# Kernel optimization log

Hardware: AMD Instinct MI355X
Metric: run time of the kernel (lower is better)

## Reference

```python
import jax, jax.numpy as jnp
import numpy as np

B, T, C, H = 4, 4096, 1024, 64

def setup_inputs() -> dict:
    key = jax.random.key(0)
    k1, k2, k3, k4 = jax.random.split(key, 4)
    x = jax.random.normal(k1, (B, T, C), dtype=jnp.float32)
    # Linear(n_embed, head_size, bias=False), stored as [in, out] for x @ W
    s = 1.0 / np.sqrt(C)
    Wq = jax.random.uniform(k2, (C, H), dtype=jnp.float32, minval=-s, maxval=s)
    Wk = jax.random.uniform(k3, (C, H), dtype=jnp.float32, minval=-s, maxval=s)
    Wv = jax.random.uniform(k4, (C, H), dtype=jnp.float32, minval=-s, maxval=s)
    return {"x": x, "Wq": Wq, "Wk": Wk, "Wv": Wv}

def reference(x, Wq, Wk, Wv):
    Bn, Tn, Cn = x.shape
    q = x @ Wq  # [B,T,H]
    k = x @ Wk  # [B,T,H]
    v = x @ Wv  # [B,T,H]
    # NOTE: original scales by C**-0.5 (embedding dim), not head_size**-0.5
    wei = jnp.einsum('bqh,bkh->bqk', q, k) * (Cn ** -0.5)  # [B,T,T]
    causal = jnp.tril(jnp.ones((Tn, Tn), dtype=bool))
    wei = jnp.where(causal, wei, -jnp.inf)
    wei = jax.nn.softmax(wei, axis=-1)
    out = jnp.einsum('bqk,bkh->bqh', wei, v)  # [B,T,H]
    return out
```

## Files before the change

### kernel.cpp

```cpp
#include <hip/hip_runtime.h>
#include <hip/hip_bf16.h>


#define B_DIM 4
#define T_DIM 4096
#define C_DIM 1024
#define H_DIM 64
#define SCALE 0.03125f
#define KP 72

typedef __attribute__((ext_vector_type(8))) short bf8;
typedef __attribute__((ext_vector_type(4))) float f32x4;

__device__ __forceinline__ ushort f2bf(float f) {
    union { float f; uint u; } x; x.f = f;
    const uint u = x.u;
    return (ushort)((u + 0x7FFFu + ((u >> 16) & 1u)) >> 16);
}
__device__ __forceinline__ uint cvt_pk_bf16(float lo, float hi) {
    uint r;
    asm("v_cvt_pk_bf16_f32 %0, %1, %2" : "=v"(r) : "v"(lo), "v"(hi));
    return r;
}

__global__ __launch_bounds__(256) void wt_kernel(
    const float* __restrict__ Wq, const float* __restrict__ Wk,
    const float* __restrict__ Wv, ushort* __restrict__ wtg)
{
    const int id  = blockIdx.x * 256 + threadIdx.x;
    const int col = id >> 7;
    const int k8  = (id & 127) * 8;
    const int m   = col >> 6, lc = col & 63;
    const float* W = (m == 0) ? Wq : (m == 1) ? Wk : Wv;
    ushort o[8];
    #pragma unroll
    for (int i = 0; i < 8; ++i)
        o[i] = f2bf(W[(size_t)(k8 + i) * H_DIM + lc]);
    *(bf8*)&wtg[(size_t)col * C_DIM + k8] = *(bf8*)o;
}

__global__ __launch_bounds__(256) void qkv_mfma_kernel(
    const float* __restrict__ x, const ushort* __restrict__ wtg,
    ushort* __restrict__ qo, ushort* __restrict__ ko, ushort* __restrict__ vo)
{
    __shared__ ushort xs[64][KP];
    __shared__ ushort wts[192][KP];
    const int t    = threadIdx.x;
    const int lane = t & 63, wave = t >> 6;
    const int g    = lane >> 4, lid = lane & 15;
    const int wr   = wave >> 1, wc = wave & 1;
    const size_t r0 = (size_t)blockIdx.x * 64;

    f32x4 acc[2][6] = {};

    const int xrow = t >> 2, xcol = (t & 3) * 16;
    float4 xr[4];
    bf8 wreg[6];

    #pragma unroll
    for (int i = 0; i < 4; ++i)
        xr[i] = *(const float4*)&x[(r0 + xrow) * C_DIM + xcol + i * 4];
    #pragma unroll
    for (int it = 0; it < 6; ++it) {
        const int n = t + it * 256;
        wreg[it] = *(const bf8*)&wtg[(size_t)(n >> 3) * C_DIM + (n & 7) * 8];
    }

    for (int kc = 0; kc < C_DIM / 64; ++kc) {
        __syncthreads();
        {
            uint p[8];
            p[0] = cvt_pk_bf16(xr[0].x, xr[0].y); p[1] = cvt_pk_bf16(xr[0].z, xr[0].w);
            p[2] = cvt_pk_bf16(xr[1].x, xr[1].y); p[3] = cvt_pk_bf16(xr[1].z, xr[1].w);
            p[4] = cvt_pk_bf16(xr[2].x, xr[2].y); p[5] = cvt_pk_bf16(xr[2].z, xr[2].w);
            p[6] = cvt_pk_bf16(xr[3].x, xr[3].y); p[7] = cvt_pk_bf16(xr[3].z, xr[3].w);
            *(bf8*)&xs[xrow][xcol]     = *(bf8*)&p[0];
            *(bf8*)&xs[xrow][xcol + 8] = *(bf8*)&p[4];
            #pragma unroll
            for (int it = 0; it < 6; ++it) {
                const int n = t + it * 256;
                *(bf8*)&wts[n >> 3][(n & 7) * 8] = wreg[it];
            }
        }
        __syncthreads();
        if (kc + 1 < C_DIM / 64) {
            const int kb = (kc + 1) * 64;
            #pragma unroll
            for (int i = 0; i < 4; ++i)
                xr[i] = *(const float4*)&x[(r0 + xrow) * C_DIM + kb + xcol + i * 4];
            #pragma unroll
            for (int it = 0; it < 6; ++it) {
                const int n = t + it * 256;
                wreg[it] = *(const bf8*)&wtg[(size_t)(n >> 3) * C_DIM + kb + (n & 7) * 8];
            }
        }
        #pragma unroll
        for (int ks = 0; ks < 2; ++ks) {
            const bf8 a0 = *(const bf8*)&xs[wr * 32 + lid][ks * 32 + g * 8];
            const bf8 a1 = *(const bf8*)&xs[wr * 32 + 16 + lid][ks * 32 + g * 8];
            #pragma unroll
            for (int j = 0; j < 6; ++j) {
                const bf8 bb = *(const bf8*)&wts[(wc * 6 + j) * 16 + lid][ks * 32 + g * 8];
                acc[0][j] = __builtin_amdgcn_mfma_f32_16x16x32_bf16(a0, bb, acc[0][j], 0, 0, 0);
                acc[1][j] = __builtin_amdgcn_mfma_f32_16x16x32_bf16(a1, bb, acc[1][j], 0, 0, 0);
            }
        }
    }

    #pragma unroll
    for (int rt = 0; rt < 2; ++rt)
        #pragma unroll
        for (int j = 0; j < 6; ++j) {
            const int ct = wc * 6 + j;
            const int m  = ct >> 2, lc = (ct & 3) * 16 + lid;
            ushort* dst = (m == 0) ? qo : (m == 1) ? ko : vo;
            const float sc = (m == 0) ? SCALE : 1.f;
            #pragma unroll
            for (int r = 0; r < 4; ++r) {
                const size_t row = r0 + wr * 32 + rt * 16 + 4 * g + r;
                dst[row * H_DIM + lc] = f2bf(acc[rt][j][r] * sc);
            }
        }
}

__global__ __launch_bounds__(256) void flash_mfma_kernel(
    const ushort* __restrict__ q, const ushort* __restrict__ k,
    const ushort* __restrict__ v, float* __restrict__ pO,
    float* __restrict__ pm, float* __restrict__ pl,
    float* __restrict__ out, int S, int nslots, int direct)
{
    const int qt = 63 - blockIdx.y;
    const int c  = blockIdx.x;
    const int kt_begin = c * S;
    const int kt_end   = min((c + 1) * S, qt + 1);
    if (kt_begin >= kt_end) return;

    __shared__ ushort ks[64][KP];
    __shared__ ushort vt[64][KP];
    __shared__ ushort ps[4][16][KP];

    const int t    = threadIdx.x;
    const int lane = t & 63, wave = t >> 6;
    const int g    = lane >> 4, lid = lane & 15;
    const int b    = blockIdx.z;
    const int bq0  = qt * 64;
    const size_t base = (size_t)b * T_DIM * H_DIM;

    const size_t qoff = base + (size_t)(bq0 + wave * 16 + lid) * H_DIM;
    const bf8 qf0 = *(const bf8*)&q[qoff + g * 8];
    const bf8 qf1 = *(const bf8*)&q[qoff + 32 + g * 8];

    f32x4 o_acc[4] = {};
    float m_run = -1e30f, l_run = 0.f;

    const int krow = t >> 3, kcol = (t & 7) * 8;
    const int vj = (t & 31) * 2, vc = (t >> 5) * 8;
    bf8 kr0, kr1, vr0, vr1;
    {
        const int kg = kt_begin * 64;
        kr0 = *(const bf8*)&k[base + (size_t)(kg + krow) * H_DIM + kcol];
        kr1 = *(const bf8*)&k[base + (size_t)(kg + 32 + krow) * H_DIM + kcol];
        vr0 = *(const bf8*)&v[base + (size_t)(kg + vj) * H_DIM + vc];
        vr1 = *(const bf8*)&v[base + (size_t)(kg + vj + 1) * H_DIM + vc];
    }

    for (int kt64 = kt_begin; kt64 < kt_end; ++kt64) {
        __syncthreads();
        *(bf8*)&ks[krow][kcol]      = kr0;
        *(bf8*)&ks[32 + krow][kcol] = kr1;
        #pragma unroll
        for (int i = 0; i < 8; ++i) {
            const uint pk = (uint)(ushort)vr0[i] | ((uint)(ushort)vr1[i] << 16);
            *(uint*)&vt[vc + i][vj] = pk;
        }
        __syncthreads();
        if (kt64 + 1 < kt_end) {
            const int kg = (kt64 + 1) * 64;
            kr0 = *(const bf8*)&k[base + (size_t)(kg + krow) * H_DIM + kcol];
            kr1 = *(const bf8*)&k[base + (size_t)(kg + 32 + krow) * H_DIM + kcol];
            vr0 = *(const bf8*)&v[base + (size_t)(kg + vj) * H_DIM + vc];
            vr1 = *(const bf8*)&v[base + (size_t)(kg + vj + 1) * H_DIM + vc];
        }

        f32x4 st[4];
        #pragma unroll
        for (int kt = 0; kt < 4; ++kt) {
            const bf8 kf0 = *(const bf8*)&ks[kt * 16 + lid][g * 8];
            const bf8 kf1 = *(const bf8*)&ks[kt * 16 + lid][32 + g * 8];
            f32x4 a = {0.f, 0.f, 0.f, 0.f};
            a = __builtin_amdgcn_mfma_f32_16x16x32_bf16(kf0, qf0, a, 0, 0, 0);
            a = __builtin_amdgcn_mfma_f32_16x16x32_bf16(kf1, qf1, a, 0, 0, 0);
            st[kt] = a;
        }

        if (kt64 == qt) {
            const int qloc = wave * 16 + lid;
            #pragma unroll
            for (int kt = 0; kt < 4; ++kt)
                #pragma unroll
                for (int r = 0; r < 4; ++r)
                    if (kt * 16 + 4 * g + r > qloc) st[kt][r] = -1e30f;
        }

        float mx0 = fmaxf(fmaxf(st[0][0], st[0][1]), fmaxf(st[0][2], st[0][3]));
        float mx1 = fmaxf(fmaxf(st[1][0], st[1][1]), fmaxf(st[1][2], st[1][3]));
        float mx2 = fmaxf(fmaxf(st[2][0], st[2][1]), fmaxf(st[2][2], st[2][3]));
        float mx3 = fmaxf(fmaxf(st[3][0], st[3][1]), fmaxf(st[3][2], st[3][3]));
        float mx = fmaxf(fmaxf(mx0, mx1), fmaxf(mx2, mx3));
        mx = fmaxf(mx, __shfl_xor(mx, 16));
        mx = fmaxf(mx, __shfl_xor(mx, 32));
        const float mnew = fmaxf(m_run, mx);
        const float fsc  = __expf(m_run - mnew);
        m_run = mnew;
        float ls = 0.f;
        #pragma unroll
        for (int kt = 0; kt < 4; ++kt)
            #pragma unroll
            for (int r = 0; r < 4; ++r) {
                const float p = __expf(st[kt][r] - mnew);
                st[kt][r] = p;
                ls += p;
            }
        ls += __shfl_xor(ls, 16);
        ls += __shfl_xor(ls, 32);
        l_run = l_run * fsc + ls;

        #pragma unroll
        for (int kt = 0; kt < 4; ++kt) {
            uint2 w;
            w.x = cvt_pk_bf16(st[kt][0], st[kt][1]);
            w.y = cvt_pk_bf16(st[kt][2], st[kt][3]);
            *(uint2*)&ps[wave][lid][kt * 16 + 4 * g] = w;
        }

        float fb[4];
        #pragma unroll
        for (int r = 0; r < 4; ++r) fb[r] = __shfl(fsc, 4 * g + r);
        #pragma unroll
        for (int ht = 0; ht < 4; ++ht)
            #pragma unroll
            for (int r = 0; r < 4; ++r) o_acc[ht][r] *= fb[r];

        const bf8 pa0 = *(const bf8*)&ps[wave][lid][g * 8];
        const bf8 pa1 = *(const bf8*)&ps[wave][lid][32 + g * 8];
        #pragma unroll
        for (int ht = 0; ht < 4; ++ht) {
            const bf8 vb0 = *(const bf8*)&vt[ht * 16 + lid][g * 8];
            const bf8 vb1 = *(const bf8*)&vt[ht * 16 + lid][32 + g * 8];
            o_acc[ht] = __builtin_amdgcn_mfma_f32_16x16x32_bf16(pa0, vb0, o_acc[ht], 0, 0, 0);
            o_acc[ht] = __builtin_amdgcn_mfma_f32_16x16x32_bf16(pa1, vb1, o_acc[ht], 0, 0, 0);
        }
    }

    if (direct) {
        float linv[4];
        #pragma unroll
        for (int r = 0; r < 4; ++r) linv[r] = 1.f / __shfl(l_run, 4 * g + r);
        #pragma unroll
        for (int r = 0; r < 4; ++r) {
            const size_t rowoff = base + (size_t)(bq0 + wave * 16 + 4 * g + r) * H_DIM;
            #pragma unroll
            for (int ht = 0; ht < 4; ++ht)
                out[rowoff + ht * 16 + lid] = o_acc[ht][r] * linv[r];
        }
    } else {
        const size_t u = ((size_t)b * 64 + qt) * nslots + c;
        #pragma unroll
        for (int r = 0; r < 4; ++r) {
            const int row = wave * 16 + 4 * g + r;
            #pragma unroll
            for (int ht = 0; ht < 4; ++ht)
                pO[u * 4096 + (size_t)row * 64 + ht * 16 + lid] = o_acc[ht][r];
        }
        if (g == 0) {
            pm[u * 64 + wave * 16 + lid] = m_run;
            pl[u * 64 + wave * 16 + lid] = l_run;
        }
    }
}

__global__ __launch_bounds__(256) void combine_kernel(
    const float* __restrict__ pO, const float* __restrict__ pm,
    const float* __restrict__ pl, float* __restrict__ out,
    int S, int nslots)
{
    const int qt = blockIdx.x, b = blockIdx.y;
    const int nch = min(nslots, (qt + S) / S);
    const int t = threadIdx.x;
    const int row = t >> 2, seg = (t & 3) * 16;
    const size_t u0 = ((size_t)b * 64 + qt) * nslots;

    float M = -1e30f;
    for (int c = 0; c < nch; ++c)
        M = fmaxf(M, pm[(u0 + c) * 64 + row]);
    float L = 0.f, alpha[8];
    for (int c = 0; c < nch; ++c) {
        alpha[c] = __expf(pm[(u0 + c) * 64 + row] - M);
        L += pl[(u0 + c) * 64 + row] * alpha[c];
    }
    const float inv = 1.f / L;

    float4 o[4] = {};
    for (int c = 0; c < nch; ++c) {
        const float a = alpha[c];
        #pragma unroll
        for (int j = 0; j < 4; ++j) {
            const float4 p = *(const float4*)&pO[(u0 + c) * 4096 +
                                                 (size_t)row * 64 + seg + j * 4];
            o[j].x += p.x * a; o[j].y += p.y * a;
            o[j].z += p.z * a; o[j].w += p.w * a;
        }
    }
    const size_t ob = (size_t)b * T_DIM * H_DIM + (size_t)(qt * 64 + row) * H_DIM + seg;
    #pragma unroll
    for (int j = 0; j < 4; ++j) {
        float4 r;
        r.x = o[j].x * inv; r.y = o[j].y * inv;
        r.z = o[j].z * inv; r.w = o[j].w * inv;
        *(float4*)&out[ob + j * 4] = r;
    }
}

extern "C" void kernel_launch(void* const* d_in, const int* in_sizes, int n_in,
                              void* d_out, int out_size, void* d_ws, size_t ws_size,
                              hipStream_t stream)
{
    const float* x  = (const float*)d_in[0];
    const float* Wq = (const float*)d_in[1];
    const float* Wk = (const float*)d_in[2];
    const float* Wv = (const float*)d_in[3];
    float* out = (float*)d_out;

    const size_t MB = 1u << 20;
    char* ws = (char*)d_ws;
    ushort* qb  = (ushort*)(ws);
    ushort* kb  = (ushort*)(ws + 2 * MB);
    ushort* vb  = (ushort*)(ws + 4 * MB);
    ushort* wtg = (ushort*)(ws + 6 * MB);
    float*  pO  = (float*)(ws + 7 * MB);

    int nslots, S;
    if      (ws_size >= 41 * MB) { nslots = 8; S = 8;  }
    else if (ws_size >= 24 * MB) { nslots = 4; S = 16; }
    else if (ws_size >= 16 * MB) { nslots = 2; S = 32; }
    else                         { nslots = 1; S = 64; }
    const int direct = (nslots == 1);
    float* pm = pO + (size_t)nslots * 1048576;
    float* pl = pm + (size_t)nslots * 16384;

    hipLaunchKernelGGL(wt_kernel, dim3(96), dim3(256), 0, stream, Wq, Wk, Wv, wtg);
    hipLaunchKernelGGL(qkv_mfma_kernel, dim3((B_DIM * T_DIM) / 64), dim3(256),
                       0, stream, x, wtg, qb, kb, vb);
    hipLaunchKernelGGL(flash_mfma_kernel, dim3(nslots, 64, B_DIM), dim3(256),
                       0, stream, qb, kb, vb, pO, pm, pl, out, S, nslots, direct);
    if (!direct)
        hipLaunchKernelGGL(combine_kernel, dim3(64, B_DIM), dim3(256),
                           0, stream, pO, pm, pl, out, S, nslots);
}
```

Baseline: 83.27 us.

## Split QKV projection per matrix, halve flash query tile, load K to registers

The QKV projection now runs one block per 64 rows per output matrix (grid y=3), which triples the block count and reduces per-block accumulator state. The flash kernel switches to 32-row query tiles with 128 threads and 128 tiles per batch. K fragments are loaded directly from global memory into registers instead of staged through LDS. It also adds a lazy rescale that skips the output rescale when the running max grows by at most 8, and the combine kernel is adapted to the new tile size. The trade-offs are that x is reread three times, K is fetched once per wave from global memory rather than shared through LDS, and the lazy-max threshold could affect numerical range.

```diff
diff --git a/kernel.cpp b/kernel.cpp
--- a/kernel.cpp
+++ b/kernel.cpp
@@ -44,27 +44,28 @@
     ushort* __restrict__ qo, ushort* __restrict__ ko, ushort* __restrict__ vo)
 {
     __shared__ ushort xs[64][KP];
-    __shared__ ushort wts[192][KP];
+    __shared__ ushort wls[64][KP];
     const int t    = threadIdx.x;
     const int lane = t & 63, wave = t >> 6;
     const int g    = lane >> 4, lid = lane & 15;
-    const int wr   = wave >> 1, wc = wave & 1;
+    const int wr32 = (wave >> 1) * 32, wc32 = (wave & 1) * 32;
+    const int m    = blockIdx.y;
     const size_t r0 = (size_t)blockIdx.x * 64;
-
-    f32x4 acc[2][6] = {};
-
-    const int xrow = t >> 2, xcol = (t & 3) * 16;
+    ushort* dst = (m == 0) ? qo : (m == 1) ? ko : vo;
+    const float sc = (m == 0) ? SCALE : 1.f;
+    const ushort* wcol = wtg + (size_t)m * 64 * C_DIM;
+
+    const int srow = t >> 2, scol = (t & 3) * 16;
+
+    f32x4 acc[2][2] = {};
     float4 xr[4];
-    bf8 wreg[6];
+    bf8 wr_[2];
 
     #pragma unroll
     for (int i = 0; i < 4; ++i)
-        xr[i] = *(const float4*)&x[(r0 + xrow) * C_DIM + xcol + i * 4];
-    #pragma unroll
-    for (int it = 0; it < 6; ++it) {
-        const int n = t + it * 256;
-        wreg[it] = *(const bf8*)&wtg[(size_t)(n >> 3) * C_DIM + (n & 7) * 8];
-    }
+        xr[i] = *(const float4*)&x[(r0 + srow) * C_DIM + scol + i * 4];
+    wr_[0] = *(const bf8*)&wcol[(size_t)srow * C_DIM + scol];
+    wr_[1] = *(const bf8*)&wcol[(size_t)srow * C_DIM + scol + 8];
 
     for (int kc = 0; kc < C_DIM / 64; ++kc) {
         __syncthreads();
@@ -74,76 +75,65 @@
             p[2] = cvt_pk_bf16(xr[1].x, xr[1].y); p[3] = cvt_pk_bf16(xr[1].z, xr[1].w);
             p[4] = cvt_pk_bf16(xr[2].x, xr[2].y); p[5] = cvt_pk_bf16(xr[2].z, xr[2].w);
             p[6] = cvt_pk_bf16(xr[3].x, xr[3].y); p[7] = cvt_pk_bf16(xr[3].z, xr[3].w);
-            *(bf8*)&xs[xrow][xcol]     = *(bf8*)&p[0];
-            *(bf8*)&xs[xrow][xcol + 8] = *(bf8*)&p[4];
-            #pragma unroll
-            for (int it = 0; it < 6; ++it) {
-                const int n = t + it * 256;
-                *(bf8*)&wts[n >> 3][(n & 7) * 8] = wreg[it];
-            }
+            *(bf8*)&xs[srow][scol]     = *(bf8*)&p[0];
+            *(bf8*)&xs[srow][scol + 8] = *(bf8*)&p[4];
+            *(bf8*)&wls[srow][scol]     = wr_[0];
+            *(bf8*)&wls[srow][scol + 8] = wr_[1];
         }
         __syncthreads();
         if (kc + 1 < C_DIM / 64) {
             const int kb = (kc + 1) * 64;
             #pragma unroll
             for (int i = 0; i < 4; ++i)
-                xr[i] = *(const float4*)&x[(r0 + xrow) * C_DIM + kb + xcol + i * 4];
-            #pragma unroll
-            for (int it = 0; it < 6; ++it) {
-                const int n = t + it * 256;
-                wreg[it] = *(const bf8*)&wtg[(size_t)(n >> 3) * C_DIM + kb + (n & 7) * 8];
-            }
+                xr[i] = *(const float4*)&x[(r0 + srow) * C_DIM + kb + scol + i * 4];
+            wr_[0] = *(const bf8*)&wcol[(size_t)srow * C_DIM + kb + scol];
+            wr_[1] = *(const bf8*)&wcol[(size_t)srow * C_DIM + kb + scol + 8];
         }
         #pragma unroll
         for (int ks = 0; ks < 2; ++ks) {
-            const bf8 a0 = *(const bf8*)&xs[wr * 32 + lid][ks * 32 + g * 8];
-            const bf8 a1 = *(const bf8*)&xs[wr * 32 + 16 + lid][ks * 32 + g * 8];
-            #pragma unroll
-            for (int j = 0; j < 6; ++j) {
-                const bf8 bb = *(const bf8*)&wts[(wc * 6 + j) * 16 + lid][ks * 32 + g * 8];
-                acc[0][j] = __builtin_amdgcn_mfma_f32_16x16x32_bf16(a0, bb, acc[0][j], 0, 0, 0);
-                acc[1][j] = __builtin_amdgcn_mfma_f32_16x16x32_bf16(a1, bb, acc[1][j], 0, 0, 0);
-            }
+            const bf8 a0 = *(const bf8*)&xs[wr32 + lid][ks * 32 + g * 8];
+            const bf8 a1 = *(const bf8*)&xs[wr32 + 16 + lid][ks * 32 + g * 8];
+            const bf8 b0 = *(const bf8*)&wls[wc32 + lid][ks * 32 + g * 8];
+            const bf8 b1 = *(const bf8*)&wls[wc32 + 16 + lid][ks * 32 + g * 8];
+            acc[0][0] = __builtin_amdgcn_mfma_f32_16x16x32_bf16(a0, b0, acc[0][0], 0, 0, 0);
+            acc[0][1] = __builtin_amdgcn_mfma_f32_16x16x32_bf16(a0, b1, acc[0][1], 0, 0, 0);
+            acc[1][0] = __builtin_amdgcn_mfma_f32_16x16x32_bf16(a1, b0, acc[1][0], 0, 0, 0);
+            acc[1][1] = __builtin_amdgcn_mfma_f32_16x16x32_bf16(a1, b1, acc[1][1], 0, 0, 0);
         }
     }
 
     #pragma unroll
     for (int rt = 0; rt < 2; ++rt)
         #pragma unroll
-        for (int j = 0; j < 6; ++j) {
-            const int ct = wc * 6 + j;
-            const int m  = ct >> 2, lc = (ct & 3) * 16 + lid;
-            ushort* dst = (m == 0) ? qo : (m == 1) ? ko : vo;
-            const float sc = (m == 0) ? SCALE : 1.f;
+        for (int ct = 0; ct < 2; ++ct)
             #pragma unroll
             for (int r = 0; r < 4; ++r) {
-                const size_t row = r0 + wr * 32 + rt * 16 + 4 * g + r;
-                dst[row * H_DIM + lc] = f2bf(acc[rt][j][r] * sc);
+                const size_t row = r0 + wr32 + rt * 16 + 4 * g + r;
+                dst[row * H_DIM + wc32 + ct * 16 + lid] = f2bf(acc[rt][ct][r] * sc);
             }
-        }
-}
-
-__global__ __launch_bounds__(256) void flash_mfma_kernel(
+}
+
+__global__ __launch_bounds__(128) void flash_mfma_kernel(
     const ushort* __restrict__ q, const ushort* __restrict__ k,
     const ushort* __restrict__ v, float* __restrict__ pO,
     float* __restrict__ pm, float* __restrict__ pl,
     float* __restrict__ out, int S, int nslots, int direct)
 {
-    const int qt = 63 - blockIdx.y;
+    const int qt = 127 - blockIdx.y;
     const int c  = blockIdx.x;
+    const int nkt_total = (qt >> 1) + 1;
     const int kt_begin = c * S;
-    const int kt_end   = min((c + 1) * S, qt + 1);
+    const int kt_end   = min((c + 1) * S, nkt_total);
     if (kt_begin >= kt_end) return;
 
-    __shared__ ushort ks[64][KP];
     __shared__ ushort vt[64][KP];
-    __shared__ ushort ps[4][16][KP];
+    __shared__ ushort ps[2][16][KP];
 
     const int t    = threadIdx.x;
     const int lane = t & 63, wave = t >> 6;
     const int g    = lane >> 4, lid = lane & 15;
     const int b    = blockIdx.z;
-    const int bq0  = qt * 64;
+    const int bq0  = qt * 32;
     const size_t base = (size_t)b * T_DIM * H_DIM;
 
     const size_t qoff = base + (size_t)(bq0 + wave * 16 + lid) * H_DIM;
@@ -153,48 +143,53 @@
     f32x4 o_acc[4] = {};
     float m_run = -1e30f, l_run = 0.f;
 
-    const int krow = t >> 3, kcol = (t & 7) * 8;
-    const int vj = (t & 31) * 2, vc = (t >> 5) * 8;
-    bf8 kr0, kr1, vr0, vr1;
+    const int vj = (t & 15) * 4, vc = (t >> 4) * 8;
+    bf8 vr[4];
     {
         const int kg = kt_begin * 64;
-        kr0 = *(const bf8*)&k[base + (size_t)(kg + krow) * H_DIM + kcol];
-        kr1 = *(const bf8*)&k[base + (size_t)(kg + 32 + krow) * H_DIM + kcol];
-        vr0 = *(const bf8*)&v[base + (size_t)(kg + vj) * H_DIM + vc];
-        vr1 = *(const bf8*)&v[base + (size_t)(kg + vj + 1) * H_DIM + vc];
+        #pragma unroll
+        for (int i = 0; i < 4; ++i)
+            vr[i] = *(const bf8*)&v[base + (size_t)(kg + vj + i) * H_DIM + vc];
     }
 
     for (int kt64 = kt_begin; kt64 < kt_end; ++kt64) {
+        const int kg0 = kt64 * 64;
+
+        bf8 kf0[4], kf1[4];
+        #pragma unroll
+        for (int kt = 0; kt < 4; ++kt) {
+            const size_t koff = base + (size_t)(kg0 + kt * 16 + lid) * H_DIM;
+            kf0[kt] = *(const bf8*)&k[koff + g * 8];
+            kf1[kt] = *(const bf8*)&k[koff + 32 + g * 8];
+        }
+
         __syncthreads();
-        *(bf8*)&ks[krow][kcol]      = kr0;
-        *(bf8*)&ks[32 + krow][kcol] = kr1;
         #pragma unroll
         for (int i = 0; i < 8; ++i) {
-            const uint pk = (uint)(ushort)vr0[i] | ((uint)(ushort)vr1[i] << 16);
-            *(uint*)&vt[vc + i][vj] = pk;
+            uint2 w;
+            w.x = (uint)(ushort)vr[0][i] | ((uint)(ushort)vr[1][i] << 16);
+            w.y = (uint)(ushort)vr[2][i] | ((uint)(ushort)vr[3][i] << 16);
+            *(uint2*)&vt[vc + i][vj] = w;
         }
         __syncthreads();
         if (kt64 + 1 < kt_end) {
             const int kg = (kt64 + 1) * 64;
-            kr0 = *(const bf8*)&k[base + (size_t)(kg + krow) * H_DIM + kcol];
-            kr1 = *(const bf8*)&k[base + (size_t)(kg + 32 + krow) * H_DIM + kcol];
-            vr0 = *(const bf8*)&v[base + (size_t)(kg + vj) * H_DIM + vc];
-            vr1 = *(const bf8*)&v[base + (size_t)(kg + vj + 1) * H_DIM + vc];
+            #pragma unroll
+            for (int i = 0; i < 4; ++i)
+                vr[i] = *(const bf8*)&v[base + (size_t)(kg + vj + i) * H_DIM + vc];
         }
 
         f32x4 st[4];
         #pragma unroll
         for (int kt = 0; kt < 4; ++kt) {
-            const bf8 kf0 = *(const bf8*)&ks[kt * 16 + lid][g * 8];
-            const bf8 kf1 = *(const bf8*)&ks[kt * 16 + lid][32 + g * 8];
             f32x4 a = {0.f, 0.f, 0.f, 0.f};
-            a = __builtin_amdgcn_mfma_f32_16x16x32_bf16(kf0, qf0, a, 0, 0, 0);
-            a = __builtin_amdgcn_mfma_f32_16x16x32_bf16(kf1, qf1, a, 0, 0, 0);
+            a = __builtin_amdgcn_mfma_f32_16x16x32_bf16(kf0[kt], qf0, a, 0, 0, 0);
+            a = __builtin_amdgcn_mfma_f32_16x16x32_bf16(kf1[kt], qf1, a, 0, 0, 0);
             st[kt] = a;
         }
 
-        if (kt64 == qt) {
-            const int qloc = wave * 16 + lid;
+        if (kt64 == (qt >> 1)) {
+            const int qloc = wave * 16 + lid + ((qt & 1) ? 32 : 0);
             #pragma unroll
             for (int kt = 0; kt < 4; ++kt)
                 #pragma unroll
@@ -202,15 +197,15 @@
                     if (kt * 16 + 4 * g + r > qloc) st[kt][r] = -1e30f;
         }
 
-        float mx0 = fmaxf(fmaxf(st[0][0], st[0][1]), fmaxf(st[0][2], st[0][3]));
-        float mx1 = fmaxf(fmaxf(st[1][0], st[1][1]), fmaxf(st[1][2], st[1][3]));
-        float mx2 = fmaxf(fmaxf(st[2][0], st[2][1]), fmaxf(st[2][2], st[2][3]));
-        float mx3 = fmaxf(fmaxf(st[3][0], st[3][1]), fmaxf(st[3][2], st[3][3]));
-        float mx = fmaxf(fmaxf(mx0, mx1), fmaxf(mx2, mx3));
+        float mx = fmaxf(fmaxf(fmaxf(st[0][0], st[0][1]), fmaxf(st[0][2], st[0][3])),
+                   fmaxf(fmaxf(fmaxf(st[1][0], st[1][1]), fmaxf(st[1][2], st[1][3])),
+                   fmaxf(fmaxf(fmaxf(st[2][0], st[2][1]), fmaxf(st[2][2], st[2][3])),
+                         fmaxf(fmaxf(st[3][0], st[3][1]), fmaxf(st[3][2], st[3][3])))));
         mx = fmaxf(mx, __shfl_xor(mx, 16));
         mx = fmaxf(mx, __shfl_xor(mx, 32));
-        const float mnew = fmaxf(m_run, mx);
-        const float fsc  = __expf(m_run - mnew);
+        const int nof = (mx <= m_run + 8.0f);
+        const float mnew = nof ? m_run : fmaxf(m_run, mx);
+        const float fsc  = nof ? 1.0f : __expf(m_run - mnew);
         m_run = mnew;
         float ls = 0.f;
         #pragma unroll
@@ -233,13 +228,15 @@
             *(uint2*)&ps[wave][lid][kt * 16 + 4 * g] = w;
         }
 
-        float fb[4];
-        #pragma unroll
-        for (int r = 0; r < 4; ++r) fb[r] = __shfl(fsc, 4 * g + r);
-        #pragma unroll
-        for (int ht = 0; ht < 4; ++ht)
-            #pragma unroll
-            for (int r = 0; r < 4; ++r) o_acc[ht][r] *= fb[r];
+        if (!__all(fsc == 1.0f)) {
+            float fb[4];
+            #pragma unroll
+            for (int r = 0; r < 4; ++r) fb[r] = __shfl(fsc, 4 * g + r);
+            #pragma unroll
+            for (int ht = 0; ht < 4; ++ht)
+                #pragma unroll
+                for (int r = 0; r < 4; ++r) o_acc[ht][r] *= fb[r];
+        }
 
         const bf8 pa0 = *(const bf8*)&ps[wave][lid][g * 8];
         const bf8 pa1 = *(const bf8*)&ps[wave][lid][32 + g * 8];
@@ -264,17 +261,17 @@
                 out[rowoff + ht * 16 + lid] = o_acc[ht][r] * linv[r];
         }
     } else {
-        const size_t u = ((size_t)b * 64 + qt) * nslots + c;
+        const size_t u = ((size_t)b * 128 + qt) * nslots + c;
         #pragma unroll
         for (int r = 0; r < 4; ++r) {
             const int row = wave * 16 + 4 * g + r;
             #pragma unroll
             for (int ht = 0; ht < 4; ++ht)
-                pO[u * 4096 + (size_t)row * 64 + ht * 16 + lid] = o_acc[ht][r];
+                pO[u * 2048 + (size_t)row * 64 + ht * 16 + lid] = o_acc[ht][r];
         }
         if (g == 0) {
-            pm[u * 64 + wave * 16 + lid] = m_run;
-            pl[u * 64 + wave * 16 + lid] = l_run;
+            pm[u * 32 + wave * 16 + lid] = m_run;
+            pl[u * 32 + wave * 16 + lid] = l_run;
         }
     }
 }
@@ -285,35 +282,36 @@
     int S, int nslots)
 {
     const int qt = blockIdx.x, b = blockIdx.y;
-    const int nch = min(nslots, (qt + S) / S);
+    const int nkt_total = (qt >> 1) + 1;
+    const int nch = (nkt_total + S - 1) / S;
     const int t = threadIdx.x;
-    const int row = t >> 2, seg = (t & 3) * 16;
-    const size_t u0 = ((size_t)b * 64 + qt) * nslots;
+    const int row = t >> 3, seg = (t & 7) * 8;
+    const size_t u0 = ((size_t)b * 128 + qt) * nslots;
 
     float M = -1e30f;
     for (int c = 0; c < nch; ++c)
-        M = fmaxf(M, pm[(u0 + c) * 64 + row]);
+        M = fmaxf(M, pm[(u0 + c) * 32 + row]);
     float L = 0.f, alpha[8];
     for (int c = 0; c < nch; ++c) {
-        alpha[c] = __expf(pm[(u0 + c) * 64 + row] - M);
-        L += pl[(u0 + c) * 64 + row] * alpha[c];
+        alpha[c] = __expf(pm[(u0 + c) * 32 + row] - M);
+        L += pl[(u0 + c) * 32 + row] * alpha[c];
     }
     const float inv = 1.f / L;
 
-    float4 o[4] = {};
+    float4 o[2] = {};
     for (int c = 0; c < nch; ++c) {
         const float a = alpha[c];
         #pragma unroll
-        for (int j = 0; j < 4; ++j) {
-            const float4 p = *(const float4*)&pO[(u0 + c) * 4096 +
+        for (int j = 0; j < 2; ++j) {
+            const float4 p = *(const float4*)&pO[(u0 + c) * 2048 +
                                                  (size_t)row * 64 + seg + j * 4];
             o[j].x += p.x * a; o[j].y += p.y * a;
             o[j].z += p.z * a; o[j].w += p.w * a;
         }
     }
-    const size_t ob = (size_t)b * T_DIM * H_DIM + (size_t)(qt * 64 + row) * H_DIM + seg;
+    const size_t ob = (size_t)b * T_DIM * H_DIM + (size_t)(qt * 32 + row) * H_DIM + seg;
     #pragma unroll
-    for (int j = 0; j < 4; ++j) {
+    for (int j = 0; j < 2; ++j) {
         float4 r;
         r.x = o[j].x * inv; r.y = o[j].y * inv;
         r.z = o[j].z * inv; r.w = o[j].w * inv;
@@ -349,11 +347,11 @@
     float* pl = pm + (size_t)nslots * 16384;
 
     hipLaunchKernelGGL(wt_kernel, dim3(96), dim3(256), 0, stream, Wq, Wk, Wv, wtg);
-    hipLaunchKernelGGL(qkv_mfma_kernel, dim3((B_DIM * T_DIM) / 64), dim3(256),
+    hipLaunchKernelGGL(qkv_mfma_kernel, dim3((B_DIM * T_DIM) / 64, 3), dim3(256),
                        0, stream, x, wtg, qb, kb, vb);
-    hipLaunchKernelGGL(flash_mfma_kernel, dim3(nslots, 64, B_DIM), dim3(256),
+    hipLaunchKernelGGL(flash_mfma_kernel, dim3(nslots, 128, B_DIM), dim3(128),
                        0, stream, qb, kb, vb, pO, pm, pl, out, S, nslots, direct);
     if (!direct)
-        hipLaunchKernelGGL(combine_kernel, dim3(64, B_DIM), dim3(256),
+        hipLaunchKernelGGL(combine_kernel, dim3(128, B_DIM), dim3(256),
                            0, stream, pO, pm, pl, out, S, nslots);
 }
```

Result: slower. 127.9 us (+53.6%).

## Use exp2 softmax with folded log2e scale, lazy rescale, smaller QKV tiles

Applied to the files above, without the earlier changes.

Folds log2(e) into the Q scaling constant so the softmax can call the hardware exp2 directly instead of __expf. It also skips the running-max update and output rescale while the new max stays within a threshold of the old one, which removes per-tile multiplies in the common case. Separately, the QKV projection kernel now uses 32-row tiles instead of 64, doubling the grid and giving each wave three column tiles. The exp2 path in combine must stay consistent with the log2-domain pm values. Smaller projection tiles reload the weight slab twice as often per row of output.

```diff
diff --git a/kernel.cpp b/kernel.cpp
--- a/kernel.cpp
+++ b/kernel.cpp
@@ -6,12 +6,15 @@
 #define T_DIM 4096
 #define C_DIM 1024
 #define H_DIM 64
-#define SCALE 0.03125f
+#define SCALE2 0.0450842066f
 #define KP 72
 
 typedef __attribute__((ext_vector_type(8))) short bf8;
 typedef __attribute__((ext_vector_type(4))) float f32x4;
 
+__device__ __forceinline__ float fast_exp2(float f) {
+    return __builtin_amdgcn_exp2f(f);
+}
 __device__ __forceinline__ ushort f2bf(float f) {
     union { float f; uint u; } x; x.f = f;
     const uint u = x.u;
@@ -43,23 +46,21 @@
     const float* __restrict__ x, const ushort* __restrict__ wtg,
     ushort* __restrict__ qo, ushort* __restrict__ ko, ushort* __restrict__ vo)
 {
-    __shared__ ushort xs[64][KP];
+    __shared__ ushort xs[32][KP];
     __shared__ ushort wts[192][KP];
     const int t    = threadIdx.x;
     const int lane = t & 63, wave = t >> 6;
     const int g    = lane >> 4, lid = lane & 15;
-    const int wr   = wave >> 1, wc = wave & 1;
-    const size_t r0 = (size_t)blockIdx.x * 64;
-
-    f32x4 acc[2][6] = {};
-
-    const int xrow = t >> 2, xcol = (t & 3) * 16;
-    float4 xr[4];
+    const size_t r0 = (size_t)blockIdx.x * 32;
+
+    f32x4 acc[2][3] = {};
+
+    const int xrow = t >> 3, xcol = (t & 7) * 8;
+    float4 xr[2];
     bf8 wreg[6];
 
-    #pragma unroll
-    for (int i = 0; i < 4; ++i)
-        xr[i] = *(const float4*)&x[(r0 + xrow) * C_DIM + xcol + i * 4];
+    xr[0] = *(const float4*)&x[(r0 + xrow) * C_DIM + xcol];
+    xr[1] = *(const float4*)&x[(r0 + xrow) * C_DIM + xcol + 4];
     #pragma unroll
     for (int it = 0; it < 6; ++it) {
         const int n = t + it * 256;
@@ -69,13 +70,10 @@
     for (int kc = 0; kc < C_DIM / 64; ++kc) {
         __syncthreads();
         {
-            uint p[8];
+            uint p[4];
             p[0] = cvt_pk_bf16(xr[0].x, xr[0].y); p[1] = cvt_pk_bf16(xr[0].z, xr[0].w);
             p[2] = cvt_pk_bf16(xr[1].x, xr[1].y); p[3] = cvt_pk_bf16(xr[1].z, xr[1].w);
-            p[4] = cvt_pk_bf16(xr[2].x, xr[2].y); p[5] = cvt_pk_bf16(xr[2].z, xr[2].w);
-            p[6] = cvt_pk_bf16(xr[3].x, xr[3].y); p[7] = cvt_pk_bf16(xr[3].z, xr[3].w);
-            *(bf8*)&xs[xrow][xcol]     = *(bf8*)&p[0];
-            *(bf8*)&xs[xrow][xcol + 8] = *(bf8*)&p[4];
+            *(bf8*)&xs[xrow][xcol] = *(bf8*)p;
             #pragma unroll
             for (int it = 0; it < 6; ++it) {
                 const int n = t + it * 256;
@@ -85,9 +83,8 @@
         __syncthreads();
         if (kc + 1 < C_DIM / 64) {
             const int kb = (kc + 1) * 64;
-            #pragma unroll
-            for (int i = 0; i < 4; ++i)
-                xr[i] = *(const float4*)&x[(r0 + xrow) * C_DIM + kb + xcol + i * 4];
+            xr[0] = *(const float4*)&x[(r0 + xrow) * C_DIM + kb + xcol];
+            xr[1] = *(const float4*)&x[(r0 + xrow) * C_DIM + kb + xcol + 4];
             #pragma unroll
             for (int it = 0; it < 6; ++it) {
                 const int n = t + it * 256;
@@ -96,11 +93,12 @@
         }
         #pragma unroll
         for (int ks = 0; ks < 2; ++ks) {
-            const bf8 a0 = *(const bf8*)&xs[wr * 32 + lid][ks * 32 + g * 8];
-            const bf8 a1 = *(const bf8*)&xs[wr * 32 + 16 + lid][ks * 32 + g * 8];
-            #pragma unroll
-            for (int j = 0; j < 6; ++j) {
-                const bf8 bb = *(const bf8*)&wts[(wc * 6 + j) * 16 + lid][ks * 32 + g * 8];
+            const bf8 a0 = *(const bf8*)&xs[lid][ks * 32 + g * 8];
+            const bf8 a1 = *(const bf8*)&xs[16 + lid][ks * 32 + g * 8];
+            #pragma unroll
+            for (int j = 0; j < 3; ++j) {
+                const int ct = wave * 3 + j;
+                const bf8 bb = *(const bf8*)&wts[ct * 16 + lid][ks * 32 + g * 8];
                 acc[0][j] = __builtin_amdgcn_mfma_f32_16x16x32_bf16(a0, bb, acc[0][j], 0, 0, 0);
                 acc[1][j] = __builtin_amdgcn_mfma_f32_16x16x32_bf16(a1, bb, acc[1][j], 0, 0, 0);
             }
@@ -110,14 +108,14 @@
     #pragma unroll
     for (int rt = 0; rt < 2; ++rt)
         #pragma unroll
-        for (int j = 0; j < 6; ++j) {
-            const int ct = wc * 6 + j;
+        for (int j = 0; j < 3; ++j) {
+            const int ct = wave * 3 + j;
             const int m  = ct >> 2, lc = (ct & 3) * 16 + lid;
             ushort* dst = (m == 0) ? qo : (m == 1) ? ko : vo;
-            const float sc = (m == 0) ? SCALE : 1.f;
+            const float sc = (m == 0) ? SCALE2 : 1.f;
             #pragma unroll
             for (int r = 0; r < 4; ++r) {
-                const size_t row = r0 + wr * 32 + rt * 16 + 4 * g + r;
+                const size_t row = r0 + rt * 16 + 4 * g + r;
                 dst[row * H_DIM + lc] = f2bf(acc[rt][j][r] * sc);
             }
         }
@@ -202,22 +200,22 @@
                     if (kt * 16 + 4 * g + r > qloc) st[kt][r] = -1e30f;
         }
 
-        float mx0 = fmaxf(fmaxf(st[0][0], st[0][1]), fmaxf(st[0][2], st[0][3]));
-        float mx1 = fmaxf(fmaxf(st[1][0], st[1][1]), fmaxf(st[1][2], st[1][3]));
-        float mx2 = fmaxf(fmaxf(st[2][0], st[2][1]), fmaxf(st[2][2], st[2][3]));
-        float mx3 = fmaxf(fmaxf(st[3][0], st[3][1]), fmaxf(st[3][2], st[3][3]));
-        float mx = fmaxf(fmaxf(mx0, mx1), fmaxf(mx2, mx3));
+        float mx = fmaxf(fmaxf(fmaxf(st[0][0], st[0][1]), fmaxf(st[0][2], st[0][3])),
+                   fmaxf(fmaxf(fmaxf(st[1][0], st[1][1]), fmaxf(st[1][2], st[1][3])),
+                   fmaxf(fmaxf(fmaxf(st[2][0], st[2][1]), fmaxf(st[2][2], st[2][3])),
+                         fmaxf(fmaxf(st[3][0], st[3][1]), fmaxf(st[3][2], st[3][3])))));
         mx = fmaxf(mx, __shfl_xor(mx, 16));
         mx = fmaxf(mx, __shfl_xor(mx, 32));
-        const float mnew = fmaxf(m_run, mx);
-        const float fsc  = __expf(m_run - mnew);
+        const bool nof = (mx <= m_run + 8.0f);
+        const float mnew = nof ? m_run : mx;
+        const float fsc  = nof ? 1.0f : fast_exp2(m_run - mnew);
         m_run = mnew;
         float ls = 0.f;
         #pragma unroll
         for (int kt = 0; kt < 4; ++kt)
             #pragma unroll
             for (int r = 0; r < 4; ++r) {
-                const float p = __expf(st[kt][r] - mnew);
+                const float p = fast_exp2(st[kt][r] - mnew);
                 st[kt][r] = p;
                 ls += p;
             }
@@ -233,13 +231,15 @@
             *(uint2*)&ps[wave][lid][kt * 16 + 4 * g] = w;
         }
 
-        float fb[4];
-        #pragma unroll
-        for (int r = 0; r < 4; ++r) fb[r] = __shfl(fsc, 4 * g + r);
-        #pragma unroll
-        for (int ht = 0; ht < 4; ++ht)
-            #pragma unroll
-            for (int r = 0; r < 4; ++r) o_acc[ht][r] *= fb[r];
+        if (!__all(nof)) {
+            float fb[4];
+            #pragma unroll
+            for (int r = 0; r < 4; ++r) fb[r] = __shfl(fsc, 4 * g + r);
+            #pragma unroll
+            for (int ht = 0; ht < 4; ++ht)
+                #pragma unroll
+                for (int r = 0; r < 4; ++r) o_acc[ht][r] *= fb[r];
+        }
 
         const bf8 pa0 = *(const bf8*)&ps[wave][lid][g * 8];
         const bf8 pa1 = *(const bf8*)&ps[wave][lid][32 + g * 8];
@@ -295,7 +295,7 @@
         M = fmaxf(M, pm[(u0 + c) * 64 + row]);
     float L = 0.f, alpha[8];
     for (int c = 0; c < nch; ++c) {
-        alpha[c] = __expf(pm[(u0 + c) * 64 + row] - M);
+        alpha[c] = fast_exp2(pm[(u0 + c) * 64 + row] - M);
         L += pl[(u0 + c) * 64 + row] * alpha[c];
     }
     const float inv = 1.f / L;
@@ -349,7 +349,7 @@
     float* pl = pm + (size_t)nslots * 16384;
 
     hipLaunchKernelGGL(wt_kernel, dim3(96), dim3(256), 0, stream, Wq, Wk, Wv, wtg);
-    hipLaunchKernelGGL(qkv_mfma_kernel, dim3((B_DIM * T_DIM) / 64), dim3(256),
+    hipLaunchKernelGGL(qkv_mfma_kernel, dim3((B_DIM * T_DIM) / 32), dim3(256),
                        0, stream, x, wtg, qb, kb, vb);
     hipLaunchKernelGGL(flash_mfma_kernel, dim3(nslots, 64, B_DIM), dim3(256),
                        0, stream, qb, kb, vb, pO, pm, pl, out, S, nslots, direct);
```

Measured after the change: 77.16 us. 7.3% less time.
